# Kernel optimization log

Measured on AMD Instinct MI355X. Metric: run time of the kernel, lower is better.

## Reference

```python
import jax, jax.numpy as jnp
import numpy as np

D = 1024  # input_size == context_size

def setup_inputs() -> dict:
    key = jax.random.key(0)
    ks = jax.random.split(key, 8)
    B, S = 16, 4096
    s = 1.0 / np.sqrt(D)
    return {
        "x": jax.random.normal(ks[0], (B, S, D), dtype=jnp.float32),
        "context": jax.random.normal(ks[1], (B, D), dtype=jnp.float32),
        "W_in": jax.random.uniform(ks[2], (D, D), jnp.float32, -s, s),
        "b_in": jax.random.uniform(ks[3], (D,), jnp.float32, -s, s),
        "W_ctx": jax.random.uniform(ks[4], (D, D), jnp.float32, -s, s),
        "b_ctx": jax.random.uniform(ks[5], (D,), jnp.float32, -s, s),
        "w_att": jax.random.uniform(ks[6], (D,), jnp.float32, -s, s),
        "b_att": jax.random.uniform(ks[7], (), jnp.float32, -s, s),
    }

def reference(x, context, W_in, b_in, W_ctx, b_ctx, w_att, b_att):
    # projected_input: [B,S,D]; projected_context: [B,D] broadcast over S
    pi = jnp.einsum('bsd,ed->bse', x, W_in) + b_in
    pc = jnp.einsum('bd,ed->be', context, W_ctx) + b_ctx
    h = jnp.tanh(pi + pc[:, None, :])                      # [B,S,D]
    scores = jnp.einsum('bsd,d->bs', h, w_att) + b_att      # [B,S]
    weights = jax.nn.softmax(scores, axis=1)                # [B,S]
    context_vector = jnp.einsum('bs,bsd->bd', weights, x)   # [B,D]
    # dropout is identity in eval mode
    return context_vector
```

## Files before the change

### kernel.cpp

```cpp
#include <hip/hip_runtime.h>
#include <hip/hip_bf16.h>
#include <math.h>

#define NB 16
#define NS 4096
#define ND 1024
#define NM (NB * NS)

#define WS_T       0
#define WS_SCORES  16384
#define WS_WEIGHTS (WS_SCORES + NB * NS)
#define WS_SHARED  (WS_WEIGHTS + NB * NS)
#define WS_XBF16   (WS_SHARED + 524288)
#define WS_SPART   (WS_XBF16 + 33554432)
#define WS_NEED    (((size_t)WS_SPART + 524288) * 4)

typedef short v8s __attribute__((ext_vector_type(8)));
typedef float v4f __attribute__((ext_vector_type(4)));
typedef unsigned short ushort;

#define G_AS __attribute__((address_space(1)))
#define L_AS __attribute__((address_space(3)))

__device__ __forceinline__ ushort f2bf(float f) {
    __hip_bfloat16 h = __float2bfloat16(f);
    return *reinterpret_cast<ushort*>(&h);
}

__device__ __forceinline__ float bf2f(ushort u) {
    return __uint_as_float(((unsigned)u) << 16);
}

__device__ __forceinline__ float fast_tanh(float x) {
    float e = __expf(2.0f * x);
    return 1.0f - 2.0f / (e + 1.0f);
}

__global__ __launch_bounds__(256) void convw_kernel(const float* __restrict__ W,
                                                    ushort* __restrict__ Wb) {
    int flat = blockIdx.x * 256 + threadIdx.x;
#pragma unroll
    for (int j = 0; j < 2; ++j) {
        int idx = flat + j * 131072;
        float4 v = ((const float4*)W)[idx];
        ushort4 o;
        o.x = f2bf(v.x); o.y = f2bf(v.y); o.z = f2bf(v.z); o.w = f2bf(v.w);
        ((ushort4*)Wb)[idx] = o;
    }
}

__global__ __launch_bounds__(256) void convx_kernel(const float* __restrict__ x,
                                                    ushort* __restrict__ xb) {
    size_t base = (size_t)blockIdx.x * 256 + threadIdx.x;
#pragma unroll
    for (int i = 0; i < 16; ++i) {
        size_t idx8 = base + (size_t)i * 524288;
        float4 a = ((const float4*)x)[idx8 * 2];
        float4 c = ((const float4*)x)[idx8 * 2 + 1];
        v8s o;
        o[0] = (short)f2bf(a.x); o[1] = (short)f2bf(a.y);
        o[2] = (short)f2bf(a.z); o[3] = (short)f2bf(a.w);
        o[4] = (short)f2bf(c.x); o[5] = (short)f2bf(c.y);
        o[6] = (short)f2bf(c.z); o[7] = (short)f2bf(c.w);
        ((v8s*)xb)[idx8] = o;
    }
}

__global__ __launch_bounds__(256) void tvec_kernel(const float* __restrict__ context,
                                                   const float* __restrict__ W_ctx,
                                                   const float* __restrict__ b_in,
                                                   const float* __restrict__ b_ctx,
                                                   float* __restrict__ t) {
    __shared__ float ctx[ND];
    int b = blockIdx.y;
    int tid = threadIdx.x;
    for (int i = tid; i < ND; i += 256) ctx[i] = context[b * ND + i];
    __syncthreads();
    int e = blockIdx.x * 64 + (tid >> 2);
    int kq = tid & 3;
    const float4* wr = (const float4*)(W_ctx + (size_t)e * ND + kq * 256);
    const float4* cr = (const float4*)(ctx + kq * 256);
    float acc = 0.f;
#pragma unroll 4
    for (int k = 0; k < 64; ++k) {
        float4 w = wr[k];
        float4 c = cr[k];
        acc += c.x * w.x + c.y * w.y + c.z * w.z + c.w * w.w;
    }
    acc += __shfl_xor(acc, 1);
    acc += __shfl_xor(acc, 2);
    if (kq == 0) t[b * ND + e] = acc + b_in[e] + b_ctx[e];
}

__global__ __launch_bounds__(512) void scores_tile_kernel(const ushort* __restrict__ xbf,
                                                          const ushort* __restrict__ Wb,
                                                          const float* __restrict__ t,
                                                          const float* __restrict__ w_att,
                                                          float* __restrict__ spart) {
    __shared__ ushort As[4][8192];
    __shared__ ushort Bs[4][8192];
    __shared__ float red[8][128];

    int tid = threadIdx.x;
    int o = blockIdx.x;
    int xcd = o & 7, idx = o >> 3;
    int ct = idx & 3;
    int rt = xcd * 32 + (idx >> 2);
    int row0 = rt << 8;
    int e0 = ct << 8;
    int b = row0 >> 12;

    const ushort* gaA0 = xbf + (size_t)(row0 + (tid >> 2)) * ND + (tid & 3) * 8;
    const ushort* gaA1 = gaA0 + (size_t)128 * ND;
    const ushort* gaB0 = Wb + (size_t)(e0 + (tid >> 2)) * ND + (tid & 3) * 8;
    const ushort* gaB1 = gaB0 + (size_t)128 * ND;

    int wid = tid >> 6, l = tid & 63;
    int l15 = l & 15, kq4 = l >> 4;
    int WM = (wid >> 2) * 128;
    int WN = (wid & 3) * 64;

    v4f acc[8][4];
#pragma unroll
    for (int i = 0; i < 8; ++i)
#pragma unroll
        for (int j = 0; j < 4; ++j) acc[i][j] = (v4f)(0.f);

#define STAGE(BUF, KO)                                                                                                 \
    {                                                                                                                  \
        __builtin_amdgcn_global_load_lds((const G_AS void*)(gaA0 + (KO)), (L_AS void*)&As[BUF][tid * 8], 16, 0, 0);    \
        __builtin_amdgcn_global_load_lds((const G_AS void*)(gaA1 + (KO)), (L_AS void*)&As[BUF][(tid + 512) * 8], 16, 0, 0); \
        __builtin_amdgcn_global_load_lds((const G_AS void*)(gaB0 + (KO)), (L_AS void*)&Bs[BUF][tid * 8], 16, 0, 0);    \
        __builtin_amdgcn_global_load_lds((const G_AS void*)(gaB1 + (KO)), (L_AS void*)&Bs[BUF][(tid + 512) * 8], 16, 0, 0); \
    }

#define COMPUTE(BUF)                                                                              \
    {                                                                                             \
        v8s bf[4];                                                                                \
        _Pragma("unroll") for (int nf = 0; nf < 4; ++nf)                                          \
            bf[nf] = *(const v8s*)&Bs[BUF][((WN + nf * 16 + l15) * 4 + kq4) * 8];                 \
        _Pragma("unroll") for (int g = 0; g < 2; ++g) {                                           \
            v8s af[4];                                                                            \
            _Pragma("unroll") for (int j = 0; j < 4; ++j)                                         \
                af[j] = *(const v8s*)&As[BUF][((WM + (g * 4 + j) * 16 + l15) * 4 + kq4) * 8];     \
            _Pragma("unroll") for (int j = 0; j < 4; ++j)                                         \
                _Pragma("unroll") for (int nf = 0; nf < 4; ++nf)                                  \
                    acc[g * 4 + j][nf] = __builtin_amdgcn_mfma_f32_16x16x32_bf16(                 \
                        af[j], bf[nf], acc[g * 4 + j][nf], 0, 0, 0);                              \
        }                                                                                         \
    }

#define KSTEP(KT, BUF, STBUF, VMTOK, DOST)                           \
    {                                                                \
        __builtin_amdgcn_s_barrier();                                \
        if (DOST) STAGE(STBUF, ((KT) + 3) * 32);                     \
        asm volatile("s_waitcnt vmcnt(" VMTOK ")" ::: "memory");     \
        __builtin_amdgcn_s_barrier();                                \
        asm volatile("" ::: "memory");                               \
        COMPUTE(BUF);                                                \
    }

    STAGE(0, 0);
    STAGE(1, 32);
    STAGE(2, 64);
    asm volatile("s_waitcnt vmcnt(8)" ::: "memory");
    __builtin_amdgcn_s_barrier();

    for (int tt = 0; tt < 7; ++tt) {
        KSTEP(4 * tt + 0, 0, 3, "12", true);
        KSTEP(4 * tt + 1, 1, 0, "12", true);
        KSTEP(4 * tt + 2, 2, 1, "12", true);
        KSTEP(4 * tt + 3, 3, 2, "12", true);
    }
    KSTEP(28, 0, 3, "12", true);
    KSTEP(29, 1, 0, "8", false);
    KSTEP(30, 2, 0, "4", false);
    KSTEP(31, 3, 0, "0", false);

#undef KSTEP
#undef COMPUTE
#undef STAGE

    float s[8][4];
#pragma unroll
    for (int i = 0; i < 8; ++i)
#pragma unroll
        for (int j = 0; j < 4; ++j) s[i][j] = 0.f;

#pragma unroll
    for (int nf = 0; nf < 4; ++nf) {
        int e = e0 + WN + nf * 16 + l15;
        float tv = t[b * ND + e];
        float wv = w_att[e];
#pragma unroll
        for (int mf = 0; mf < 8; ++mf)
#pragma unroll
            for (int r = 0; r < 4; ++r)
                s[mf][r] += fast_tanh(acc[mf][nf][r] + tv) * wv;
    }
#pragma unroll
    for (int mf = 0; mf < 8; ++mf)
#pragma unroll
        for (int r = 0; r < 4; ++r) {
            float v = s[mf][r];
            v += __shfl_xor(v, 1);
            v += __shfl_xor(v, 2);
            v += __shfl_xor(v, 4);
            v += __shfl_xor(v, 8);
            s[mf][r] = v;
        }
    if (l15 == 0) {
#pragma unroll
        for (int mf = 0; mf < 8; ++mf)
#pragma unroll
            for (int r = 0; r < 4; ++r)
                red[wid][mf * 16 + kq4 * 4 + r] = s[mf][r];
    }
    __syncthreads();
    if (tid < 256) {
        int mg = tid >> 7;
        int rl = tid & 127;
        float v = red[mg * 4 + 0][rl] + red[mg * 4 + 1][rl] +
                  red[mg * 4 + 2][rl] + red[mg * 4 + 3][rl];
        spart[ct * 65536 + row0 + mg * 128 + rl] = v;
    }
}

__global__ __launch_bounds__(512) void scores_mfma_kernel(const float* __restrict__ x,
                                                          const ushort* __restrict__ Wb,
                                                          const float* __restrict__ t,
                                                          const float* __restrict__ w_att,
                                                          float* __restrict__ scores) {
    __shared__ ushort As[2][64 * 256];
    __shared__ float red[8][64];

    int tid = threadIdx.x;
    int row0 = blockIdx.x * 64;
    int b = row0 >> 12;
    const float4* xf4 = (const float4*)x;

    int sr = tid >> 3;
    int sc = tid & 7;
    int swzbase = (sr & 7) << 3;

    float4 nx[8];
#pragma unroll
    for (int j = 0; j < 8; ++j)
        nx[j] = xf4[(size_t)(row0 + sr) * 256 + sc + j * 8];
#pragma unroll
    for (int j = 0; j < 8; ++j) {
        int c4 = sc + j * 8;
        ushort4 o;
        o.x = f2bf(nx[j].x); o.y = f2bf(nx[j].y); o.z = f2bf(nx[j].z); o.w = f2bf(nx[j].w);
        *(ushort4*)&As[0][sr * 256 + ((c4 * 4) ^ swzbase)] = o;
    }
    __syncthreads();

    int w = tid >> 6;
    int l = tid & 63;
    int l15 = l & 15;
    int kofs = (l >> 4) * 8;
    int xorv = (l & 7) << 3;
    int n0 = w * 128;

    v4f acc[2][4][4];
#pragma unroll
    for (int p = 0; p < 2; ++p)
#pragma unroll
        for (int i = 0; i < 4; ++i)
#pragma unroll
            for (int j = 0; j < 4; ++j) acc[p][i][j] = (v4f)(0.f);

    const ushort* bbase0 = Wb + (size_t)(n0 + l15) * ND + kofs;
    const ushort* bbase1 = bbase0 + (size_t)64 * ND;

#pragma unroll
    for (int kh = 0; kh < 4; ++kh) {
        if (kh < 3) {
#pragma unroll
            for (int j = 0; j < 8; ++j)
                nx[j] = xf4[(size_t)(row0 + sr) * 256 + (kh + 1) * 64 + sc + j * 8];
        }
        const ushort* Ab = &As[kh & 1][0];
        int kb = kh * 256;

        v8s b0c[4], b0n[4], b1[4];
#pragma unroll
        for (int nf = 0; nf < 4; ++nf) b0c[nf] = *(const v8s*)(bbase0 + (size_t)nf * 16 * ND + kb);

#pragma unroll
        for (int ks = 0; ks < 8; ++ks) {
            int kk = kb + ks * 32;
            int elem = (ks * 32 + kofs) ^ xorv;
            v8s af[4];
#pragma unroll
            for (int mf = 0; mf < 4; ++mf)
                af[mf] = *(const v8s*)&Ab[(mf * 16 + l15) * 256 + elem];
#pragma unroll
            for (int nf = 0; nf < 4; ++nf)
                b1[nf] = *(const v8s*)(bbase1 + (size_t)nf * 16 * ND + kk);
            if (ks < 7) {
#pragma unroll
                for (int nf = 0; nf < 4; ++nf)
                    b0n[nf] = *(const v8s*)(bbase0 + (size_t)nf * 16 * ND + kk + 32);
            }
#pragma unroll
            for (int mf = 0; mf < 4; ++mf)
#pragma unroll
                for (int nf = 0; nf < 4; ++nf)
                    acc[0][mf][nf] = __builtin_amdgcn_mfma_f32_16x16x32_bf16(
                        af[mf], b0c[nf], acc[0][mf][nf], 0, 0, 0);
#pragma unroll
            for (int mf = 0; mf < 4; ++mf)
#pragma unroll
                for (int nf = 0; nf < 4; ++nf)
                    acc[1][mf][nf] = __builtin_amdgcn_mfma_f32_16x16x32_bf16(
                        af[mf], b1[nf], acc[1][mf][nf], 0, 0, 0);
#pragma unroll
            for (int nf = 0; nf < 4; ++nf) b0c[nf] = b0n[nf];
        }

        if (kh < 3) {
#pragma unroll
            for (int j = 0; j < 8; ++j) {
                int c4 = sc + j * 8;
                ushort4 o;
                o.x = f2bf(nx[j].x); o.y = f2bf(nx[j].y); o.z = f2bf(nx[j].z); o.w = f2bf(nx[j].w);
                *(ushort4*)&As[(kh + 1) & 1][sr * 256 + ((c4 * 4) ^ swzbase)] = o;
            }
            __syncthreads();
        }
    }

    float s[4][4];
#pragma unroll
    for (int i = 0; i < 4; ++i)
#pragma unroll
        for (int j = 0; j < 4; ++j) s[i][j] = 0.f;

#pragma unroll
    for (int pass = 0; pass < 2; ++pass)
#pragma unroll
        for (int nf = 0; nf < 4; ++nf) {
            int e = n0 + pass * 64 + nf * 16 + l15;
            float tv = t[b * ND + e];
            float wv = w_att[e];
#pragma unroll
            for (int mf = 0; mf < 4; ++mf)
#pragma unroll
                for (int r = 0; r < 4; ++r)
                    s[mf][r] += fast_tanh(acc[pass][mf][nf][r] + tv) * wv;
        }

#pragma unroll
    for (int mf = 0; mf < 4; ++mf)
#pragma unroll
        for (int r = 0; r < 4; ++r) {
            float v = s[mf][r];
            v += __shfl_xor(v, 1);
            v += __shfl_xor(v, 2);
            v += __shfl_xor(v, 4);
            v += __shfl_xor(v, 8);
            s[mf][r] = v;
        }
    if (l15 == 0) {
#pragma unroll
        for (int mf = 0; mf < 4; ++mf)
#pragma unroll
            for (int r = 0; r < 4; ++r)
                red[w][mf * 16 + (l >> 4) * 4 + r] = s[mf][r];
    }
    __syncthreads();
    if (tid < 64) {
        float v = 0.f;
#pragma unroll
        for (int ww = 0; ww < 8; ++ww) v += red[ww][tid];
        scores[(size_t)b * NS + (row0 & (NS - 1)) + tid] = v;
    }
}

__global__ __launch_bounds__(256) void softmax4_kernel(const float* __restrict__ spart,
                                                       float* __restrict__ weights) {
    int b = blockIdx.x;
    int tid = threadIdx.x;
    float v[16];
    float lmax = -1e30f;
#pragma unroll
    for (int i = 0; i < 16; ++i) {
        int grow = b * NS + tid + i * 256;
        float sum = 0.f;
#pragma unroll
        for (int c = 0; c < 4; ++c) sum += spart[c * 65536 + grow];
        v[i] = sum;
        lmax = fmaxf(lmax, sum);
    }
#pragma unroll
    for (int off = 32; off >= 1; off >>= 1) lmax = fmaxf(lmax, __shfl_xor(lmax, off));
    __shared__ float redm[4];
    int wave = tid >> 6;
    if ((tid & 63) == 0) redm[wave] = lmax;
    __syncthreads();
    float bmax = fmaxf(fmaxf(redm[0], redm[1]), fmaxf(redm[2], redm[3]));

    float lsum = 0.f;
#pragma unroll
    for (int i = 0; i < 16; ++i) {
        v[i] = expf(v[i] - bmax);
        lsum += v[i];
    }
#pragma unroll
    for (int off = 32; off >= 1; off >>= 1) lsum += __shfl_xor(lsum, off);
    __shared__ float reds[4];
    if ((tid & 63) == 0) reds[wave] = lsum;
    __syncthreads();
    float inv = 1.0f / (reds[0] + reds[1] + reds[2] + reds[3]);
#pragma unroll
    for (int i = 0; i < 16; ++i) weights[b * NS + tid + i * 256] = v[i] * inv;
}

__global__ __launch_bounds__(256) void softmax_kernel(const float* __restrict__ scores,
                                                      float* __restrict__ weights) {
    int b = blockIdx.x;
    int tid = threadIdx.x;
    float v[16];
    float lmax = -1e30f;
#pragma unroll
    for (int i = 0; i < 16; ++i) {
        v[i] = scores[b * NS + tid + i * 256];
        lmax = fmaxf(lmax, v[i]);
    }
#pragma unroll
    for (int off = 32; off >= 1; off >>= 1) lmax = fmaxf(lmax, __shfl_xor(lmax, off));
    __shared__ float redm[4];
    int wave = tid >> 6;
    if ((tid & 63) == 0) redm[wave] = lmax;
    __syncthreads();
    float bmax = fmaxf(fmaxf(redm[0], redm[1]), fmaxf(redm[2], redm[3]));

    float lsum = 0.f;
#pragma unroll
    for (int i = 0; i < 16; ++i) {
        v[i] = expf(v[i] - bmax);
        lsum += v[i];
    }
#pragma unroll
    for (int off = 32; off >= 1; off >>= 1) lsum += __shfl_xor(lsum, off);
    __shared__ float reds[4];
    if ((tid & 63) == 0) reds[wave] = lsum;
    __syncthreads();
    float inv = 1.0f / (reds[0] + reds[1] + reds[2] + reds[3]);
#pragma unroll
    for (int i = 0; i < 16; ++i) weights[b * NS + tid + i * 256] = v[i] * inv;
}

__global__ __launch_bounds__(256) void wsum_kernel(const float* __restrict__ x,
                                                   const float* __restrict__ w,
                                                   float* __restrict__ part) {
    int sc = blockIdx.x, b = blockIdx.y;
    int d0 = threadIdx.x * 4;
    const float* xb = x + ((size_t)b * NS + sc * 128) * ND;
    const float* wb = w + b * NS + sc * 128;
    float4 acc = {0.f, 0.f, 0.f, 0.f};
    for (int ss = 0; ss < 128; ++ss) {
        float wv = wb[ss];
        float4 xv = *(const float4*)&xb[(size_t)ss * ND + d0];
        acc.x += wv * xv.x;
        acc.y += wv * xv.y;
        acc.z += wv * xv.z;
        acc.w += wv * xv.w;
    }
    *(float4*)&part[(size_t)(b * 32 + sc) * ND + d0] = acc;
}

__global__ __launch_bounds__(256) void wsum_bf_kernel(const ushort* __restrict__ xbf,
                                                      const float* __restrict__ w,
                                                      float* __restrict__ part) {
    int sc = blockIdx.x, b = blockIdx.y;
    int d0 = threadIdx.x * 4;
    const ushort* xb = xbf + ((size_t)b * NS + sc * 128) * ND;
    const float* wb = w + b * NS + sc * 128;
    float4 acc = {0.f, 0.f, 0.f, 0.f};
    for (int ss = 0; ss < 128; ++ss) {
        float wv = wb[ss];
        ushort4 xv = *(const ushort4*)&xb[(size_t)ss * ND + d0];
        acc.x += wv * bf2f(xv.x);
        acc.y += wv * bf2f(xv.y);
        acc.z += wv * bf2f(xv.z);
        acc.w += wv * bf2f(xv.w);
    }
    *(float4*)&part[(size_t)(b * 32 + sc) * ND + d0] = acc;
}

__global__ __launch_bounds__(256) void reduce_kernel(const float* __restrict__ part,
                                                     float* __restrict__ out) {
    int b = blockIdx.x;
    int d0 = threadIdx.x * 4;
    float4 acc = {0.f, 0.f, 0.f, 0.f};
#pragma unroll
    for (int sc = 0; sc < 32; ++sc) {
        float4 v = *(const float4*)&part[(size_t)(b * 32 + sc) * ND + d0];
        acc.x += v.x;
        acc.y += v.y;
        acc.z += v.z;
        acc.w += v.w;
    }
    *(float4*)&out[b * ND + d0] = acc;
}

extern "C" void kernel_launch(void* const* d_in, const int* in_sizes, int n_in,
                              void* d_out, int out_size, void* d_ws, size_t ws_size,
                              hipStream_t stream) {
    const float* x       = (const float*)d_in[0];
    const float* context = (const float*)d_in[1];
    const float* W_in    = (const float*)d_in[2];
    const float* b_in    = (const float*)d_in[3];
    const float* W_ctx   = (const float*)d_in[4];
    const float* b_ctx   = (const float*)d_in[5];
    const float* w_att   = (const float*)d_in[6];

    float* ws      = (float*)d_ws;
    float* t       = ws + WS_T;
    float* scores  = ws + WS_SCORES;
    float* weights = ws + WS_WEIGHTS;
    ushort* wbf16  = (ushort*)(ws + WS_SHARED);
    ushort* xbf16  = (ushort*)(ws + WS_XBF16);
    float* spart   = ws + WS_SPART;
    float* partfb  = ws + WS_SHARED;
    float* out     = (float*)d_out;

    bool fast = ws_size >= WS_NEED;

    convw_kernel<<<dim3(512), 256, 0, stream>>>(W_in, wbf16);
    tvec_kernel<<<dim3(16, NB), 256, 0, stream>>>(context, W_ctx, b_in, b_ctx, t);
    if (fast) {
        convx_kernel<<<dim3(2048), 256, 0, stream>>>(x, xbf16);
        scores_tile_kernel<<<dim3(1024), 512, 0, stream>>>(xbf16, wbf16, t, w_att, spart);
        softmax4_kernel<<<dim3(NB), 256, 0, stream>>>(spart, weights);
        wsum_bf_kernel<<<dim3(32, NB), 256, 0, stream>>>(xbf16, weights, spart);
        reduce_kernel<<<dim3(NB), 256, 0, stream>>>(spart, out);
    } else {
        scores_mfma_kernel<<<dim3(NM / 64), 512, 0, stream>>>(x, wbf16, t, w_att, scores);
        softmax_kernel<<<dim3(NB), 256, 0, stream>>>(scores, weights);
        wsum_kernel<<<dim3(32, NB), 256, 0, stream>>>(x, weights, partfb);
        reduce_kernel<<<dim3(NB), 256, 0, stream>>>(partfb, out);
    }
}
```

Baseline: 287.2 us.

## Fuse fp32-to-bf16 conversion of x into the scores GEMM and drop convx pass

Removes the separate pass that converted x to bf16 in workspace. The GEMM now stages fp32 x tiles into LDS and converts them to bf16 when building MFMA fragments, and the weighted sum reads fp32 x directly. This eliminates a full read-and-write of the large activation tensor. In exchange, A-tile global and LDS traffic doubles, conversion ALU work moves into the inner loop, and the pipeline drops from four buffers to three.

```diff
diff --git a/kernel.cpp b/kernel.cpp
--- a/kernel.cpp
+++ b/kernel.cpp
@@ -11,8 +11,7 @@
 #define WS_SCORES  16384
 #define WS_WEIGHTS (WS_SCORES + NB * NS)
 #define WS_SHARED  (WS_WEIGHTS + NB * NS)
-#define WS_XBF16   (WS_SHARED + 524288)
-#define WS_SPART   (WS_XBF16 + 33554432)
+#define WS_SPART   (WS_SHARED + 524288)
 #define WS_NEED    (((size_t)WS_SPART + 524288) * 4)
 
 typedef short v8s __attribute__((ext_vector_type(8)));
@@ -25,10 +24,6 @@
 __device__ __forceinline__ ushort f2bf(float f) {
     __hip_bfloat16 h = __float2bfloat16(f);
     return *reinterpret_cast<ushort*>(&h);
-}
-
-__device__ __forceinline__ float bf2f(ushort u) {
-    return __uint_as_float(((unsigned)u) << 16);
 }
 
 __device__ __forceinline__ float fast_tanh(float x) {
@@ -46,23 +41,6 @@
         ushort4 o;
         o.x = f2bf(v.x); o.y = f2bf(v.y); o.z = f2bf(v.z); o.w = f2bf(v.w);
         ((ushort4*)Wb)[idx] = o;
-    }
-}
-
-__global__ __launch_bounds__(256) void convx_kernel(const float* __restrict__ x,
-                                                    ushort* __restrict__ xb) {
-    size_t base = (size_t)blockIdx.x * 256 + threadIdx.x;
-#pragma unroll
-    for (int i = 0; i < 16; ++i) {
-        size_t idx8 = base + (size_t)i * 524288;
-        float4 a = ((const float4*)x)[idx8 * 2];
-        float4 c = ((const float4*)x)[idx8 * 2 + 1];
-        v8s o;
-        o[0] = (short)f2bf(a.x); o[1] = (short)f2bf(a.y);
-        o[2] = (short)f2bf(a.z); o[3] = (short)f2bf(a.w);
-        o[4] = (short)f2bf(c.x); o[5] = (short)f2bf(c.y);
-        o[6] = (short)f2bf(c.z); o[7] = (short)f2bf(c.w);
-        ((v8s*)xb)[idx8] = o;
     }
 }
 
@@ -92,13 +70,13 @@
     if (kq == 0) t[b * ND + e] = acc + b_in[e] + b_ctx[e];
 }
 
-__global__ __launch_bounds__(512) void scores_tile_kernel(const ushort* __restrict__ xbf,
+__global__ __launch_bounds__(512) void scores_tile_kernel(const float* __restrict__ x,
                                                           const ushort* __restrict__ Wb,
                                                           const float* __restrict__ t,
                                                           const float* __restrict__ w_att,
                                                           float* __restrict__ spart) {
-    __shared__ ushort As[4][8192];
-    __shared__ ushort Bs[4][8192];
+    __shared__ float Af[3][8192];
+    __shared__ ushort Bs[3][8192];
     __shared__ float red[8][128];
 
     int tid = threadIdx.x;
@@ -110,8 +88,7 @@
     int e0 = ct << 8;
     int b = row0 >> 12;
 
-    const ushort* gaA0 = xbf + (size_t)(row0 + (tid >> 2)) * ND + (tid & 3) * 8;
-    const ushort* gaA1 = gaA0 + (size_t)128 * ND;
+    const float* gA0 = x + (size_t)(row0 + (tid >> 3)) * ND + (tid & 7) * 4;
     const ushort* gaB0 = Wb + (size_t)(e0 + (tid >> 2)) * ND + (tid & 3) * 8;
     const ushort* gaB1 = gaB0 + (size_t)128 * ND;
 
@@ -126,12 +103,16 @@
 #pragma unroll
         for (int j = 0; j < 4; ++j) acc[i][j] = (v4f)(0.f);
 
-#define STAGE(BUF, KO)                                                                                                 \
-    {                                                                                                                  \
-        __builtin_amdgcn_global_load_lds((const G_AS void*)(gaA0 + (KO)), (L_AS void*)&As[BUF][tid * 8], 16, 0, 0);    \
-        __builtin_amdgcn_global_load_lds((const G_AS void*)(gaA1 + (KO)), (L_AS void*)&As[BUF][(tid + 512) * 8], 16, 0, 0); \
-        __builtin_amdgcn_global_load_lds((const G_AS void*)(gaB0 + (KO)), (L_AS void*)&Bs[BUF][tid * 8], 16, 0, 0);    \
-        __builtin_amdgcn_global_load_lds((const G_AS void*)(gaB1 + (KO)), (L_AS void*)&Bs[BUF][(tid + 512) * 8], 16, 0, 0); \
+#define STAGE(BUF, KT)                                                                              \
+    {                                                                                               \
+        _Pragma("unroll") for (int j = 0; j < 4; ++j)                                               \
+            __builtin_amdgcn_global_load_lds(                                                       \
+                (const G_AS void*)(gA0 + (size_t)j * 64 * ND + (KT) * 32),                          \
+                (L_AS void*)&Af[BUF][(tid + j * 512) * 4], 16, 0, 0);                               \
+        __builtin_amdgcn_global_load_lds((const G_AS void*)(gaB0 + (KT) * 32),                      \
+                                         (L_AS void*)&Bs[BUF][tid * 8], 16, 0, 0);                 \
+        __builtin_amdgcn_global_load_lds((const G_AS void*)(gaB1 + (KT) * 32),                      \
+                                         (L_AS void*)&Bs[BUF][(tid + 512) * 8], 16, 0, 0);         \
     }
 
 #define COMPUTE(BUF)                                                                              \
@@ -141,8 +122,17 @@
             bf[nf] = *(const v8s*)&Bs[BUF][((WN + nf * 16 + l15) * 4 + kq4) * 8];                 \
         _Pragma("unroll") for (int g = 0; g < 2; ++g) {                                           \
             v8s af[4];                                                                            \
-            _Pragma("unroll") for (int j = 0; j < 4; ++j)                                         \
-                af[j] = *(const v8s*)&As[BUF][((WM + (g * 4 + j) * 16 + l15) * 4 + kq4) * 8];     \
+            _Pragma("unroll") for (int j = 0; j < 4; ++j) {                                       \
+                int row = WM + (g * 4 + j) * 16 + l15;                                            \
+                v4f lo = *(const v4f*)&Af[BUF][(row * 8 + kq4 * 2) * 4];                          \
+                v4f hi = *(const v4f*)&Af[BUF][(row * 8 + kq4 * 2 + 1) * 4];                      \
+                v8s a;                                                                            \
+                a[0] = (short)f2bf(lo[0]); a[1] = (short)f2bf(lo[1]);                             \
+                a[2] = (short)f2bf(lo[2]); a[3] = (short)f2bf(lo[3]);                             \
+                a[4] = (short)f2bf(hi[0]); a[5] = (short)f2bf(hi[1]);                             \
+                a[6] = (short)f2bf(hi[2]); a[7] = (short)f2bf(hi[3]);                             \
+                af[j] = a;                                                                        \
+            }                                                                                     \
             _Pragma("unroll") for (int j = 0; j < 4; ++j)                                         \
                 _Pragma("unroll") for (int nf = 0; nf < 4; ++nf)                                  \
                     acc[g * 4 + j][nf] = __builtin_amdgcn_mfma_f32_16x16x32_bf16(                 \
@@ -153,7 +143,7 @@
 #define KSTEP(KT, BUF, STBUF, VMTOK, DOST)                           \
     {                                                                \
         __builtin_amdgcn_s_barrier();                                \
-        if (DOST) STAGE(STBUF, ((KT) + 3) * 32);                     \
+        if (DOST) STAGE(STBUF, (KT) + 2);                            \
         asm volatile("s_waitcnt vmcnt(" VMTOK ")" ::: "memory");     \
         __builtin_amdgcn_s_barrier();                                \
         asm volatile("" ::: "memory");                               \
@@ -161,21 +151,17 @@
     }
 
     STAGE(0, 0);
-    STAGE(1, 32);
-    STAGE(2, 64);
-    asm volatile("s_waitcnt vmcnt(8)" ::: "memory");
+    STAGE(1, 1);
+    asm volatile("s_waitcnt vmcnt(6)" ::: "memory");
     __builtin_amdgcn_s_barrier();
 
-    for (int tt = 0; tt < 7; ++tt) {
-        KSTEP(4 * tt + 0, 0, 3, "12", true);
-        KSTEP(4 * tt + 1, 1, 0, "12", true);
-        KSTEP(4 * tt + 2, 2, 1, "12", true);
-        KSTEP(4 * tt + 3, 3, 2, "12", true);
-    }
-    KSTEP(28, 0, 3, "12", true);
-    KSTEP(29, 1, 0, "8", false);
-    KSTEP(30, 2, 0, "4", false);
-    KSTEP(31, 3, 0, "0", false);
+    for (int tt = 0; tt < 10; ++tt) {
+        KSTEP(3 * tt + 0, 0, 2, "12", true);
+        KSTEP(3 * tt + 1, 1, 0, "12", true);
+        KSTEP(3 * tt + 2, 2, 1, "12", true);
+    }
+    KSTEP(30, 0, 0, "6", false);
+    KSTEP(31, 1, 0, "0", false);
 
 #undef KSTEP
 #undef COMPUTE
@@ -472,25 +458,6 @@
     *(float4*)&part[(size_t)(b * 32 + sc) * ND + d0] = acc;
 }
 
-__global__ __launch_bounds__(256) void wsum_bf_kernel(const ushort* __restrict__ xbf,
-                                                      const float* __restrict__ w,
-                                                      float* __restrict__ part) {
-    int sc = blockIdx.x, b = blockIdx.y;
-    int d0 = threadIdx.x * 4;
-    const ushort* xb = xbf + ((size_t)b * NS + sc * 128) * ND;
-    const float* wb = w + b * NS + sc * 128;
-    float4 acc = {0.f, 0.f, 0.f, 0.f};
-    for (int ss = 0; ss < 128; ++ss) {
-        float wv = wb[ss];
-        ushort4 xv = *(const ushort4*)&xb[(size_t)ss * ND + d0];
-        acc.x += wv * bf2f(xv.x);
-        acc.y += wv * bf2f(xv.y);
-        acc.z += wv * bf2f(xv.z);
-        acc.w += wv * bf2f(xv.w);
-    }
-    *(float4*)&part[(size_t)(b * 32 + sc) * ND + d0] = acc;
-}
-
 __global__ __launch_bounds__(256) void reduce_kernel(const float* __restrict__ part,
                                                      float* __restrict__ out) {
     int b = blockIdx.x;
@@ -523,7 +490,6 @@
     float* scores  = ws + WS_SCORES;
     float* weights = ws + WS_WEIGHTS;
     ushort* wbf16  = (ushort*)(ws + WS_SHARED);
-    ushort* xbf16  = (ushort*)(ws + WS_XBF16);
     float* spart   = ws + WS_SPART;
     float* partfb  = ws + WS_SHARED;
     float* out     = (float*)d_out;
@@ -533,10 +499,9 @@
     convw_kernel<<<dim3(512), 256, 0, stream>>>(W_in, wbf16);
     tvec_kernel<<<dim3(16, NB), 256, 0, stream>>>(context, W_ctx, b_in, b_ctx, t);
     if (fast) {
-        convx_kernel<<<dim3(2048), 256, 0, stream>>>(x, xbf16);
-        scores_tile_kernel<<<dim3(1024), 512, 0, stream>>>(xbf16, wbf16, t, w_att, spart);
+        scores_tile_kernel<<<dim3(1024), 512, 0, stream>>>(x, wbf16, t, w_att, spart);
         softmax4_kernel<<<dim3(NB), 256, 0, stream>>>(spart, weights);
-        wsum_bf_kernel<<<dim3(32, NB), 256, 0, stream>>>(xbf16, weights, spart);
+        wsum_kernel<<<dim3(32, NB), 256, 0, stream>>>(x, weights, spart);
         reduce_kernel<<<dim3(NB), 256, 0, stream>>>(spart, out);
     } else {
         scores_mfma_kernel<<<dim3(NM / 64), 512, 0, stream>>>(x, wbf16, t, w_att, scores);
```

Result: slower. 307.2 us (+7.0%).
